# Optimization experiments

Hardware: AMD Instinct MI355X
Metric: run time of the kernel (lower is better)

Reference implementation:

```python
import jax, jax.numpy as jnp
import numpy as np

N = 8192       # n_nodes
D = 256        # conf.unify['dim']
GAMMA = 3.0    # conf.unify['gamma']
ALPHA = 0.5    # conf.unify['alpha']
EPS = 1e-6


def setup_inputs() -> dict:
    key = jax.random.key(0)
    k1, k2, k3, k4 = jax.random.split(key, 4)
    z = jax.random.normal(k1, (N, D), dtype=jnp.float32)
    # kaiming-uniform-ish scale for W
    W = jax.random.normal(k2, (D, D), dtype=jnp.float32) * (1.0 / np.sqrt(D))
    beta = jax.random.uniform(k3, (N, 1), dtype=jnp.float32)      # beta_vector, init ~0.5
    Q = jax.random.uniform(k4, (N, N), dtype=jnp.float32)          # nonnegative prior (dense stand-in for sparse Q)
    return {"z": z, "W": W, "beta": beta, "Q": Q}


def reference(z, W, beta, Q):
    # init-time: Q row-normalized (normalize(Q, style='row'))
    Qn = Q / jnp.sum(Q, axis=1, keepdims=True)            # [N, N]

    # 1. similarity: sim = (z @ W) @ z.T
    sim = (z @ W) @ z.T                                    # [N, N]

    # 2. sparsify: relu(sim - beta), relu + eps, power 1/(gamma-1)
    adj = jax.nn.relu(sim - beta)                          # beta [N,1] broadcasts over columns
    adj = jax.nn.relu(adj) + EPS                           # relu_with_eps
    adj = adj ** (1.0 / (GAMMA - 1.0))                     # gamma power-law sparsify

    # 3. fuse Q: (1-alpha)*adj + alpha*(adj*Q), then /N
    adj = (1.0 - ALPHA) * adj + ALPHA * (adj * Qn)
    adj = adj / N

    # 4. row-normalize
    adj = adj / jnp.sum(adj, axis=-1, keepdims=True)
    return adj
```

## Files before the change

### kernel.cpp

```cpp
#include <hip/hip_runtime.h>
#include <hip/hip_bf16.h>
#include <math.h>

#define N 8192
#define D 256
#define EPSF 1e-6f

typedef __attribute__((ext_vector_type(8))) short short8v;
typedef __attribute__((ext_vector_type(4))) float f32x4;
typedef __attribute__((ext_vector_type(4))) unsigned short u16x4;

__device__ __forceinline__ unsigned short f2bf(float x) {
    __hip_bfloat16 h = __float2bfloat16(x);
    return *(unsigned short*)&h;
}
__device__ __forceinline__ float bf2f(unsigned short u) {
    __hip_bfloat16 h = *(__hip_bfloat16*)&u;
    return __bfloat162float(h);
}
__device__ __forceinline__ float bfu2f(unsigned short u) {
    unsigned int x = ((unsigned int)u) << 16;
    float f;
    __builtin_memcpy(&f, &x, 4);
    return f;
}
__device__ __forceinline__ void ntstore4(float* p, f32x4 v) {
    __builtin_nontemporal_store(v, (f32x4*)p);
}

#define GLOAD_LDS16(gp, lp)                                                                  \
    __builtin_amdgcn_global_load_lds((const __attribute__((address_space(1))) unsigned int*)(gp), \
                                     (__attribute__((address_space(3))) unsigned int*)(lp), 16, 0, 0)

__global__ __launch_bounds__(256) void split_kernel(const float* __restrict__ x,
                                                    unsigned short* __restrict__ hi,
                                                    unsigned short* __restrict__ lo) {
    int i = (blockIdx.x * 256 + threadIdx.x) * 4;
    float4 v = *(const float4*)&x[i];
    ushort4 h, l;
    float a;
    a = v.x; h.x = f2bf(a); l.x = f2bf(a - bf2f(h.x));
    a = v.y; h.y = f2bf(a); l.y = f2bf(a - bf2f(h.y));
    a = v.z; h.z = f2bf(a); l.z = f2bf(a - bf2f(h.z));
    a = v.w; h.w = f2bf(a); l.w = f2bf(a - bf2f(h.w));
    *(ushort4*)&hi[i] = h;
    *(ushort4*)&lo[i] = l;
}

__global__ __launch_bounds__(256) void zw_kernel(const float* __restrict__ z,
                                                 const float* __restrict__ W,
                                                 unsigned short* __restrict__ Ah,
                                                 unsigned short* __restrict__ Al) {
    __shared__ float zs[32 * D];
    int rowBase = blockIdx.x * 32;
    const float4* zg = (const float4*)(z + (size_t)rowBase * D);
    float4* zs4 = (float4*)zs;
    for (int i = threadIdx.x; i < 32 * D / 4; i += 256) zs4[i] = zg[i];
    __syncthreads();

    float acc[32];
#pragma unroll
    for (int r = 0; r < 32; ++r) acc[r] = 0.f;
    int col = threadIdx.x;
    for (int kb = 0; kb < D; kb += 4) {
        float w0 = W[(size_t)(kb + 0) * D + col];
        float w1 = W[(size_t)(kb + 1) * D + col];
        float w2 = W[(size_t)(kb + 2) * D + col];
        float w3 = W[(size_t)(kb + 3) * D + col];
#pragma unroll
        for (int r = 0; r < 32; ++r) {
            float4 zv = *(const float4*)&zs[r * D + kb];
            acc[r] = fmaf(zv.x, w0, acc[r]);
            acc[r] = fmaf(zv.y, w1, acc[r]);
            acc[r] = fmaf(zv.z, w2, acc[r]);
            acc[r] = fmaf(zv.w, w3, acc[r]);
        }
    }
#pragma unroll
    for (int r = 0; r < 32; ++r) {
        float a = acc[r];
        unsigned short h = f2bf(a);
        unsigned short l = f2bf(a - bf2f(h));
        Ah[(size_t)(rowBase + r) * D + col] = h;
        Al[(size_t)(rowBase + r) * D + col] = l;
    }
}

template <bool BF16S>
__global__ __launch_bounds__(512, 2) void gemm_s_kernel(
    const unsigned short* __restrict__ Ah, const unsigned short* __restrict__ Al,
    const unsigned short* __restrict__ Bh, const unsigned short* __restrict__ Bl,
    const float* __restrict__ beta, unsigned short* __restrict__ sbf,
    float* __restrict__ sf32) {
    __shared__ unsigned short lds[2][4][256][32];

    int bid = blockIdx.x;
    int xcd = bid & 7;
    int idx = bid >> 3;
    int rowIn = idx & 3;
    int bx = idx >> 2;
    int by = xcd * 4 + rowIn;
    int rowBase = by * 256;
    int colBase = bx * 256;

    int t = threadIdx.x;
    int lane = t & 63;
    int w = t >> 6;
    int wr = w >> 2, wc = w & 3;
    int fr = lane & 15;
    int fg = lane >> 4;

    int mat = w & 3;
    int half = w >> 2;
    const unsigned short* tsrc = (mat == 0) ? Ah : (mat == 1) ? Al : (mat == 2) ? Bh : Bl;
    int tRB = (mat < 2) ? rowBase : colBase;
    int slot_src = (lane & 3) ^ ((lane >> 3) & 3);
    const unsigned short* gt =
        tsrc + (size_t)(tRB + half * 128 + (lane >> 2)) * D + slot_src * 8;

    f32x4 acc[8][4];
#pragma unroll
    for (int m = 0; m < 8; ++m)
#pragma unroll
        for (int n = 0; n < 4; ++n) acc[m][n] = (f32x4){0.f, 0.f, 0.f, 0.f};

    auto stage = [&](int buf, int kt) {
#pragma unroll
        for (int j = 0; j < 8; ++j)
            GLOAD_LDS16(gt + kt + j * 16 * D, &lds[buf][mat][half * 128 + j * 16][0]);
    };

    stage(0, 0);
    int cur = 0;
    for (int kt = 0; kt < D; kt += 32) {
        __syncthreads();
        if (kt + 32 < D) stage(cur ^ 1, kt + 32);
        __builtin_amdgcn_sched_barrier(0);

        short8v bh[4], bl[4];
#pragma unroll
        for (int n = 0; n < 4; ++n) {
            int row = wc * 64 + n * 16 + fr;
            int sl = fg ^ ((fr >> 1) & 3);
            bh[n] = *(const short8v*)&lds[cur][2][row][sl * 8];
            bl[n] = *(const short8v*)&lds[cur][3][row][sl * 8];
        }
        __builtin_amdgcn_s_setprio(1);
#pragma unroll
        for (int m = 0; m < 8; ++m) {
            int row = wr * 128 + m * 16 + fr;
            int sl = fg ^ ((fr >> 1) & 3);
            short8v ah = *(const short8v*)&lds[cur][0][row][sl * 8];
            short8v al = *(const short8v*)&lds[cur][1][row][sl * 8];
#pragma unroll
            for (int n = 0; n < 4; ++n) {
                acc[m][n] = __builtin_amdgcn_mfma_f32_16x16x32_bf16(ah, bh[n], acc[m][n], 0, 0, 0);
                acc[m][n] = __builtin_amdgcn_mfma_f32_16x16x32_bf16(ah, bl[n], acc[m][n], 0, 0, 0);
                acc[m][n] = __builtin_amdgcn_mfma_f32_16x16x32_bf16(al, bh[n], acc[m][n], 0, 0, 0);
            }
        }
        __builtin_amdgcn_s_setprio(0);
        cur ^= 1;
    }

    __syncthreads();
    float* scratch = (float*)lds + w * (16 * 68);

#pragma unroll
    for (int m = 0; m < 8; ++m) {
#pragma unroll
        for (int n = 0; n < 4; ++n)
#pragma unroll
            for (int reg = 0; reg < 4; ++reg)
                scratch[(fg * 4 + reg) * 68 + n * 16 + fr] = acc[m][n][reg];

#pragma unroll
        for (int sub = 0; sub < 4; ++sub) {
            int rloc = sub * 4 + fg;
            int i = rowBase + wr * 128 + m * 16 + rloc;
            int col = colBase + wc * 64 + fr * 4;
            float4 sv = *(const float4*)&scratch[rloc * 68 + fr * 4];
            float bi = beta[i];
            float s0 = sqrtf(fmaxf(sv.x - bi, 0.f) + EPSF);
            float s1 = sqrtf(fmaxf(sv.y - bi, 0.f) + EPSF);
            float s2 = sqrtf(fmaxf(sv.z - bi, 0.f) + EPSF);
            float s3 = sqrtf(fmaxf(sv.w - bi, 0.f) + EPSF);
            if constexpr (BF16S) {
                u16x4 o = {f2bf(s0), f2bf(s1), f2bf(s2), f2bf(s3)};
                __builtin_nontemporal_store(o, (u16x4*)(sbf + (size_t)i * N + col));
            } else {
                f32x4 o = {s0, s1, s2, s3};
                ntstore4(sf32 + (size_t)i * N + col, o);
            }
        }
        __syncthreads();
    }
}

template <bool BF16S>
__global__ __launch_bounds__(512) void rownorm_kernel(float* __restrict__ out,
                                                      const float* __restrict__ Q,
                                                      const unsigned short* __restrict__ sbf) {
    __shared__ float red[24];

    int row = blockIdx.x;
    int t = threadIdx.x;
    const float* qrow = Q + (size_t)row * N;

    f32x4 qv[4];
    float sf[16];
#pragma unroll
    for (int g = 0; g < 4; ++g) {
        int e = g * 2048 + t * 4;
        qv[g] = *(const f32x4*)(qrow + e);
        if constexpr (BF16S) {
            u16x4 sp = *(const u16x4*)(sbf + (size_t)row * N + e);
            sf[g * 4 + 0] = bfu2f(sp.x);
            sf[g * 4 + 1] = bfu2f(sp.y);
            sf[g * 4 + 2] = bfu2f(sp.z);
            sf[g * 4 + 3] = bfu2f(sp.w);
        } else {
            f32x4 sv = *(const f32x4*)(out + (size_t)row * N + e);
            sf[g * 4 + 0] = sv.x;
            sf[g * 4 + 1] = sv.y;
            sf[g * 4 + 2] = sv.z;
            sf[g * 4 + 3] = sv.w;
        }
    }

    float ps = 0.f, pq = 0.f, qs = 0.f;
#pragma unroll
    for (int g = 0; g < 4; ++g)
#pragma unroll
        for (int j = 0; j < 4; ++j) {
            float q = qv[g][j];
            float s = sf[g * 4 + j];
            ps += s;
            pq += s * q;
            qs += q;
        }
#pragma unroll
    for (int off = 1; off < 64; off <<= 1) {
        ps += __shfl_xor(ps, off, 64);
        pq += __shfl_xor(pq, off, 64);
        qs += __shfl_xor(qs, off, 64);
    }
    if ((t & 63) == 0) {
        int wv = t >> 6;
        red[wv * 3 + 0] = ps;
        red[wv * 3 + 1] = pq;
        red[wv * 3 + 2] = qs;
    }
    __syncthreads();
    float tps = 0.f, tpq = 0.f, tqs = 0.f;
#pragma unroll
    for (int i = 0; i < 8; ++i) {
        tps += red[i * 3 + 0];
        tpq += red[i * 3 + 1];
        tqs += red[i * 3 + 2];
    }
    float sh = 0.5f / tqs;
    float wv = 1.0f / (0.5f * tps + sh * tpq);

    float* orow = out + (size_t)row * N;
#pragma unroll
    for (int g = 0; g < 4; ++g) {
        int e = g * 2048 + t * 4;
        f32x4 o;
#pragma unroll
        for (int j = 0; j < 4; ++j)
            o[j] = sf[g * 4 + j] * fmaf(qv[g][j], sh, 0.5f) * wv;
        ntstore4(orow + e, o);
    }
}

extern "C" void kernel_launch(void* const* d_in, const int* in_sizes, int n_in,
                              void* d_out, int out_size, void* d_ws, size_t ws_size,
                              hipStream_t stream) {
    const float* z = (const float*)d_in[0];
    const float* W = (const float*)d_in[1];
    const float* beta = (const float*)d_in[2];
    const float* Q = (const float*)d_in[3];
    float* out = (float*)d_out;

    unsigned short* Ah = (unsigned short*)d_ws;
    unsigned short* Al = Ah + (size_t)N * D;
    unsigned short* Bh = Al + (size_t)N * D;
    unsigned short* Bl = Bh + (size_t)N * D;
    unsigned short* sbf = Bl + (size_t)N * D;

    size_t need = 4 * (size_t)N * D * sizeof(unsigned short) + (size_t)N * N * sizeof(unsigned short);
    bool bf16s = (ws_size >= need);

    split_kernel<<<(N * D / 4) / 256, 256, 0, stream>>>(z, Bh, Bl);
    zw_kernel<<<N / 32, 256, 0, stream>>>(z, W, Ah, Al);
    if (bf16s) {
        gemm_s_kernel<true><<<1024, 512, 0, stream>>>(Ah, Al, Bh, Bl, beta, sbf, nullptr);
        rownorm_kernel<true><<<N, 512, 0, stream>>>(out, Q, sbf);
    } else {
        gemm_s_kernel<false><<<1024, 512, 0, stream>>>(Ah, Al, Bh, Bl, beta, nullptr, out);
        rownorm_kernel<false><<<N, 512, 0, stream>>>(out, Q, nullptr);
    }
}
```

Measured before the change: 313.4 us.

## Prefetch two K-tiles ahead with vmcnt waits; widen rownorm loads

The GEMM main loop now issues the first two K-stages up front and waits with explicit s_waitcnt vmcnt counts plus raw barriers, so one tile's global-to-LDS loads stay in flight while the other is computed. The next stage is refilled into the just-consumed buffer after a second barrier. The row-normalisation kernel switches to 16-byte bf16 loads covering 8 contiguous elements per thread, issues all loads before conversion, and adds an occupancy hint to launch bounds. The aim is to hide load latency in the GEMM and improve memory-level parallelism in the bandwidth-bound rownorm, at the cost of fragile hand-coded wait counts and an extra barrier per iteration.

```diff
diff --git a/kernel.cpp b/kernel.cpp
--- a/kernel.cpp
+++ b/kernel.cpp
@@ -131,10 +131,17 @@
     };
 
     stage(0, 0);
-    int cur = 0;
-    for (int kt = 0; kt < D; kt += 32) {
-        __syncthreads();
-        if (kt + 32 < D) stage(cur ^ 1, kt + 32);
+    stage(1, 32);
+
+    for (int kt8 = 0; kt8 < 8; ++kt8) {
+        const int cur = kt8 & 1;
+        if (kt8 < 7) {
+            asm volatile("s_waitcnt vmcnt(8)" ::: "memory");
+        } else {
+            asm volatile("s_waitcnt vmcnt(0)" ::: "memory");
+        }
+        __builtin_amdgcn_sched_barrier(0);
+        __builtin_amdgcn_s_barrier();
         __builtin_amdgcn_sched_barrier(0);
 
         short8v bh[4], bl[4];
@@ -160,7 +167,11 @@
             }
         }
         __builtin_amdgcn_s_setprio(0);
-        cur ^= 1;
+        __builtin_amdgcn_sched_barrier(0);
+        __builtin_amdgcn_s_barrier();
+        __builtin_amdgcn_sched_barrier(0);
+        if (kt8 + 2 < 8) stage(cur, (kt8 + 2) * 32);
+        __builtin_amdgcn_sched_barrier(0);
     }
 
     __syncthreads();
@@ -198,33 +209,46 @@
 }
 
 template <bool BF16S>
-__global__ __launch_bounds__(512) void rownorm_kernel(float* __restrict__ out,
-                                                      const float* __restrict__ Q,
-                                                      const unsigned short* __restrict__ sbf) {
+__global__ __launch_bounds__(512, 4) void rownorm_kernel(float* __restrict__ out,
+                                                         const float* __restrict__ Q,
+                                                         const unsigned short* __restrict__ sbf) {
     __shared__ float red[24];
 
     int row = blockIdx.x;
     int t = threadIdx.x;
     const float* qrow = Q + (size_t)row * N;
 
+    float sf[16];
     f32x4 qv[4];
-    float sf[16];
-#pragma unroll
-    for (int g = 0; g < 4; ++g) {
-        int e = g * 2048 + t * 4;
-        qv[g] = *(const f32x4*)(qrow + e);
-        if constexpr (BF16S) {
-            u16x4 sp = *(const u16x4*)(sbf + (size_t)row * N + e);
-            sf[g * 4 + 0] = bfu2f(sp.x);
-            sf[g * 4 + 1] = bfu2f(sp.y);
-            sf[g * 4 + 2] = bfu2f(sp.z);
-            sf[g * 4 + 3] = bfu2f(sp.w);
-        } else {
-            f32x4 sv = *(const f32x4*)(out + (size_t)row * N + e);
-            sf[g * 4 + 0] = sv.x;
-            sf[g * 4 + 1] = sv.y;
-            sf[g * 4 + 2] = sv.z;
-            sf[g * 4 + 3] = sv.w;
+    if constexpr (BF16S) {
+        short8v sp0 = *(const short8v*)(sbf + (size_t)row * N + t * 8);
+        short8v sp1 = *(const short8v*)(sbf + (size_t)row * N + 4096 + t * 8);
+        qv[0] = *(const f32x4*)(qrow + t * 8);
+        qv[1] = *(const f32x4*)(qrow + t * 8 + 4);
+        qv[2] = *(const f32x4*)(qrow + 4096 + t * 8);
+        qv[3] = *(const f32x4*)(qrow + 4096 + t * 8 + 4);
+        __builtin_amdgcn_sched_barrier(0);
+#pragma unroll
+        for (int j = 0; j < 8; ++j) {
+            sf[j] = bfu2f((unsigned short)sp0[j]);
+            sf[8 + j] = bfu2f((unsigned short)sp1[j]);
+        }
+    } else {
+        f32x4 sv0 = *(const f32x4*)(out + (size_t)row * N + t * 8);
+        f32x4 sv1 = *(const f32x4*)(out + (size_t)row * N + t * 8 + 4);
+        f32x4 sv2 = *(const f32x4*)(out + (size_t)row * N + 4096 + t * 8);
+        f32x4 sv3 = *(const f32x4*)(out + (size_t)row * N + 4096 + t * 8 + 4);
+        qv[0] = *(const f32x4*)(qrow + t * 8);
+        qv[1] = *(const f32x4*)(qrow + t * 8 + 4);
+        qv[2] = *(const f32x4*)(qrow + 4096 + t * 8);
+        qv[3] = *(const f32x4*)(qrow + 4096 + t * 8 + 4);
+        __builtin_amdgcn_sched_barrier(0);
+#pragma unroll
+        for (int j = 0; j < 4; ++j) {
+            sf[j] = sv0[j];
+            sf[4 + j] = sv1[j];
+            sf[8 + j] = sv2[j];
+            sf[12 + j] = sv3[j];
         }
     }
 
@@ -233,8 +257,8 @@
     for (int g = 0; g < 4; ++g)
 #pragma unroll
         for (int j = 0; j < 4; ++j) {
+            float s = sf[g * 4 + j];
             float q = qv[g][j];
-            float s = sf[g * 4 + j];
             ps += s;
             pq += s * q;
             qs += q;
@@ -263,15 +287,19 @@
     float wv = 1.0f / (0.5f * tps + sh * tpq);
 
     float* orow = out + (size_t)row * N;
-#pragma unroll
-    for (int g = 0; g < 4; ++g) {
-        int e = g * 2048 + t * 4;
-        f32x4 o;
-#pragma unroll
-        for (int j = 0; j < 4; ++j)
-            o[j] = sf[g * 4 + j] * fmaf(qv[g][j], sh, 0.5f) * wv;
-        ntstore4(orow + e, o);
-    }
+    f32x4 o;
+#pragma unroll
+    for (int j = 0; j < 4; ++j) o[j] = sf[j] * fmaf(qv[0][j], sh, 0.5f) * wv;
+    ntstore4(orow + t * 8, o);
+#pragma unroll
+    for (int j = 0; j < 4; ++j) o[j] = sf[4 + j] * fmaf(qv[1][j], sh, 0.5f) * wv;
+    ntstore4(orow + t * 8 + 4, o);
+#pragma unroll
+    for (int j = 0; j < 4; ++j) o[j] = sf[8 + j] * fmaf(qv[2][j], sh, 0.5f) * wv;
+    ntstore4(orow + 4096 + t * 8, o);
+#pragma unroll
+    for (int j = 0; j < 4; ++j) o[j] = sf[12 + j] * fmaf(qv[3][j], sh, 0.5f) * wv;
+    ntstore4(orow + 4096 + t * 8 + 4, o);
 }
 
 extern "C" void kernel_launch(void* const* d_in, const int* in_sizes, int n_in,
```

Result: slower. 410.4 us (+31.0%).
